# Performance work log

Measured on AMD Instinct MI355X. Metric: run time of the kernel, lower is better.

Reference implementation:

```python
import jax, jax.numpy as jnp
import numpy as np

NCHUNK, NBATCH, HALF = 32, 64, 128
C_SCALE, M_SCALE = 1e-4, 1e-5


def force(t):
    return jnp.sin(t)


def setup_inputs() -> dict:
    key = jax.random.key(0)
    k1, k2, k3, k4, k5 = jax.random.split(key, 5)
    t = jax.random.uniform(k1, (NCHUNK, NBATCH), dtype=jnp.float32)
    y = jax.random.normal(k2, (NCHUNK, NBATCH, 2 * HALF), dtype=jnp.float32)
    # positive stiffness / damping / mass, bounded away from zero
    K = jax.random.uniform(k3, (HALF,), dtype=jnp.float32) + 0.5
    C = jax.random.uniform(k4, (HALF,), dtype=jnp.float32) + 0.5
    M = jax.random.uniform(k5, (HALF,), dtype=jnp.float32) + 0.5
    return {"t": t, "y": y, "K": K, "C": C, "M": M}


def reference(t, y, K, C, M):
    half = K.shape[0]
    size = 2 * half
    Ms = M * M_SCALE
    Cs = C * C_SCALE

    u = y[..., :half]          # displacements (nchunk, nbatch, half)
    v = y[..., half:]          # velocities    (nchunk, nbatch, half)
    du = jnp.diff(u, axis=-1)  # (..., half-1)
    dv = jnp.diff(v, axis=-1)

    # internal force per link i: K_i*du_i + C_i*dv_i, distributed to nodes i and i+1
    f = K[:-1] * du + Cs[:-1] * dv                         # (..., half-1)
    pad = [(0, 0)] * (y.ndim - 1)
    vdot = jnp.pad(f / Ms[:-1], pad + [(0, 1)]) \
         + jnp.pad(-f / Ms[1:], pad + [(1, 0)])            # (..., half)
    vdot = vdot.at[..., -1].add(-(K[-1] * u[..., -1] + Cs[-1] * v[..., -1]) / Ms[-1])
    vdot = vdot.at[..., 0].add(force(t) / Ms[0])
    ydot = jnp.concatenate([v, vdot], axis=-1)             # (..., size)

    # Jacobian is constant over chunk/batch dims: assemble one (size,size) block matrix
    # lower-left block: d(vdot)/d(u)
    ku = jnp.diag(-K / Ms)
    ku = ku.at[1:, 1:].add(jnp.diag(-K[:-1] / Ms[1:]))
    ku = ku + jnp.diag(K[:-1] / Ms[:-1], k=1) + jnp.diag(K[:-1] / Ms[1:], k=-1)
    # lower-right block: d(vdot)/d(v)
    kv = jnp.diag(-Cs / Ms)
    kv = kv.at[1:, 1:].add(jnp.diag(-Cs[:-1] / Ms[1:]))
    kv = kv + jnp.diag(Cs[:-1] / Ms[:-1], k=1) + jnp.diag(Cs[:-1] / Ms[1:], k=-1)

    Jb = jnp.zeros((size, size), dtype=y.dtype)
    Jb = Jb.at[:half, half:].set(jnp.eye(half, dtype=y.dtype))  # d(udot)/d(v) = I
    Jb = Jb.at[half:, :half].set(ku)
    Jb = Jb.at[half:, half:].set(kv)

    J = jnp.broadcast_to(Jb, y.shape + (size,))
    return ydot, J
```

## Files before the change

kernel.cpp:

```cpp
#include <hip/hip_runtime.h>
#include <hip/hip_bf16.h>

#define NCHUNK 32
#define NBATCH 64
#define HALF   128
#define SIZE   (2 * HALF)
#define NROWS  (NCHUNK * NBATCH)
#define C_SCALE 1e-4f
#define M_SCALE 1e-5f

__global__ void jb_kernel(const float* __restrict__ K,
                          const float* __restrict__ C,
                          const float* __restrict__ M,
                          float* __restrict__ Jb) {
    int r = blockIdx.x;
    int c = threadIdx.x;
    float val = 0.0f;
    if (r < HALF) {
        val = (c == r + HALF) ? 1.0f : 0.0f;
    } else {
        int i = r - HALF;
        float Mi = M[i] * M_SCALE;
        bool isV = (c >= HALF);
        int  j   = isV ? (c - HALF) : c;
        float scale = isV ? C_SCALE : 1.0f;
        const float* __restrict__ A = isV ? C : K;
        if (j == i) {
            val = -A[i] * scale / Mi;
            if (i >= 1) val += -A[i - 1] * scale / Mi;
        } else if (j == i + 1 && i < HALF - 1) {
            val = A[i] * scale / Mi;
        } else if (j == i - 1) {
            val = A[i - 1] * scale / Mi;
        }
    }
    Jb[r * SIZE + c] = val;
}

__global__ void bcast_kernel(const float4* __restrict__ src,
                             float4* __restrict__ dst,
                             long total4) {
    long idx    = (long)blockIdx.x * blockDim.x + threadIdx.x;
    long stride = (long)gridDim.x * blockDim.x;
    for (; idx < total4; idx += stride) {
        dst[idx] = src[idx & 16383];
    }
}

__global__ void ydot_kernel(const float* __restrict__ t,
                            const float* __restrict__ y,
                            const float* __restrict__ K,
                            const float* __restrict__ C,
                            const float* __restrict__ M,
                            float* __restrict__ out) {
    int row = blockIdx.x;
    int i   = threadIdx.x;
    const float* yr = y + (long)row * SIZE;

    float u = yr[i];
    float v = yr[HALF + i];
    out[(long)row * SIZE + i] = v;

    float Mi   = M[i] * M_SCALE;
    float vdot = 0.0f;
    if (i < HALF - 1) {
        float f = K[i] * (yr[i + 1] - u) + C[i] * C_SCALE * (yr[HALF + i + 1] - v);
        vdot += f / Mi;
    }
    if (i >= 1) {
        float fm = K[i - 1] * (u - yr[i - 1]) + C[i - 1] * C_SCALE * (v - yr[HALF + i - 1]);
        vdot -= fm / Mi;
    }
    if (i == HALF - 1) {
        vdot += -(K[HALF - 1] * u + C[HALF - 1] * C_SCALE * v) / Mi;
    }
    if (i == 0) {
        vdot += sinf(t[row]) / Mi;
    }
    out[(long)row * SIZE + HALF + i] = vdot;
}

extern "C" void kernel_launch(void* const* d_in, const int* in_sizes, int n_in,
                              void* d_out, int out_size, void* d_ws, size_t ws_size,
                              hipStream_t stream) {
    const float* t = (const float*)d_in[0];
    const float* y = (const float*)d_in[1];
    const float* K = (const float*)d_in[2];
    const float* C = (const float*)d_in[3];
    const float* M = (const float*)d_in[4];

    float* out  = (float*)d_out;
    float* Jout = out + (long)NROWS * SIZE;

    jb_kernel<<<SIZE, SIZE, 0, stream>>>(K, C, M, Jout);

    const float4* src = (const float4*)Jout;
    float4*       dst = (float4*)Jout + 16384;
    long total4 = (long)(NROWS - 1) * 16384;
    bcast_kernel<<<2048, 256, 0, stream>>>(src, dst, total4);

    ydot_kernel<<<NROWS, HALF, 0, stream>>>(t, y, K, C, M, out);
}
```

Before: 538.9 us.

## Fuse Jacobian build and broadcast into one write-only kernel

Drops the separate Jb build kernel and the broadcast copy kernel. Each thread now computes its float4 of the block matrix in registers and writes it straight into 64 output copies, so the copy kernel's re-reads of the source block and one launch go away. The grid is 2048 blocks, each covering one 256-float4 slice across 64 copies, and every block recomputes the same Jb values redundantly. Division is replaced by multiplying with a reciprocal.

```diff
diff --git a/kernel.cpp b/kernel.cpp
--- a/kernel.cpp
+++ b/kernel.cpp
@@ -9,41 +9,54 @@
 #define C_SCALE 1e-4f
 #define M_SCALE 1e-5f
 
-__global__ void jb_kernel(const float* __restrict__ K,
-                          const float* __restrict__ C,
-                          const float* __restrict__ M,
-                          float* __restrict__ Jb) {
-    int r = blockIdx.x;
-    int c = threadIdx.x;
-    float val = 0.0f;
+#define JB_F4   16384
+#define COPIES_PER_GROUP 64
+
+__global__ __launch_bounds__(256) void j_kernel(const float* __restrict__ K,
+                                                const float* __restrict__ C,
+                                                const float* __restrict__ M,
+                                                float* __restrict__ Jout) {
+    int tid = threadIdx.x;
+    int b   = blockIdx.x;
+    int s   = b & 63;
+    int g   = b >> 6;
+    int o4  = s * 256 + tid;
+    int r   = o4 >> 6;
+    int c0  = (o4 & 63) << 2;
+
+    float vals[4];
     if (r < HALF) {
-        val = (c == r + HALF) ? 1.0f : 0.0f;
+        #pragma unroll
+        for (int k = 0; k < 4; ++k)
+            vals[k] = (c0 + k == r + HALF) ? 1.0f : 0.0f;
     } else {
-        int i = r - HALF;
-        float Mi = M[i] * M_SCALE;
-        bool isV = (c >= HALF);
-        int  j   = isV ? (c - HALF) : c;
-        float scale = isV ? C_SCALE : 1.0f;
-        const float* __restrict__ A = isV ? C : K;
-        if (j == i) {
-            val = -A[i] * scale / Mi;
-            if (i >= 1) val += -A[i - 1] * scale / Mi;
-        } else if (j == i + 1 && i < HALF - 1) {
-            val = A[i] * scale / Mi;
-        } else if (j == i - 1) {
-            val = A[i - 1] * scale / Mi;
+        int   i     = r - HALF;
+        float invMi = 1.0f / (M[i] * M_SCALE);
+        #pragma unroll
+        for (int k = 0; k < 4; ++k) {
+            int  c   = c0 + k;
+            bool isV = (c >= HALF);
+            int  j   = isV ? (c - HALF) : c;
+            float scale = isV ? C_SCALE : 1.0f;
+            const float* __restrict__ A = isV ? C : K;
+            float v = 0.0f;
+            if (j == i) {
+                v = -A[i] * scale * invMi;
+                if (i >= 1) v += -A[i - 1] * scale * invMi;
+            } else if (j == i + 1 && i < HALF - 1) {
+                v = A[i] * scale * invMi;
+            } else if (j == i - 1) {
+                v = A[i - 1] * scale * invMi;
+            }
+            vals[k] = v;
         }
     }
-    Jb[r * SIZE + c] = val;
-}
+    float4 val = make_float4(vals[0], vals[1], vals[2], vals[3]);
 
-__global__ void bcast_kernel(const float4* __restrict__ src,
-                             float4* __restrict__ dst,
-                             long total4) {
-    long idx    = (long)blockIdx.x * blockDim.x + threadIdx.x;
-    long stride = (long)gridDim.x * blockDim.x;
-    for (; idx < total4; idx += stride) {
-        dst[idx] = src[idx & 16383];
+    float4* dst = (float4*)Jout + (long)g * COPIES_PER_GROUP * JB_F4 + o4;
+    #pragma unroll
+    for (int cp = 0; cp < COPIES_PER_GROUP; ++cp) {
+        dst[(long)cp * JB_F4] = val;
     }
 }
 
@@ -92,12 +105,7 @@
     float* out  = (float*)d_out;
     float* Jout = out + (long)NROWS * SIZE;
 
-    jb_kernel<<<SIZE, SIZE, 0, stream>>>(K, C, M, Jout);
-
-    const float4* src = (const float4*)Jout;
-    float4*       dst = (float4*)Jout + 16384;
-    long total4 = (long)(NROWS - 1) * 16384;
-    bcast_kernel<<<2048, 256, 0, stream>>>(src, dst, total4);
+    j_kernel<<<NROWS, 256, 0, stream>>>(K, C, M, Jout);
 
     ydot_kernel<<<NROWS, HALF, 0, stream>>>(t, y, K, C, M, out);
 }
```

Result: no change. 531.2 us (-1.4%).

## Fuse Jacobian generation, broadcast and ydot into one write-only kernel

Applied to the files above, without the earlier changes.

Replaces the three launches (build one Jacobian block, copy it to every row, compute ydot) with a single kernel. Each block regenerates the 256x256 Jacobian directly in registers and writes it with vectorized nontemporal stores, so the broadcast no longer reads the source block, and ydot runs as extra blocks in the same grid. This removes the read traffic and launch overhead of the broadcast in exchange for recomputing the tridiagonal entries (with a division per row) in every block.

```diff
diff --git a/kernel.cpp b/kernel.cpp
--- a/kernel.cpp
+++ b/kernel.cpp
@@ -9,75 +9,85 @@
 #define C_SCALE 1e-4f
 #define M_SCALE 1e-5f
 
-__global__ void jb_kernel(const float* __restrict__ K,
-                          const float* __restrict__ C,
-                          const float* __restrict__ M,
-                          float* __restrict__ Jb) {
-    int r = blockIdx.x;
-    int c = threadIdx.x;
-    float val = 0.0f;
-    if (r < HALF) {
-        val = (c == r + HALF) ? 1.0f : 0.0f;
+#define JB_F4    16384
+#define JBLOCKS  NROWS
+#define YBLOCKS  (NROWS * HALF / 256)
+
+typedef float floatx4 __attribute__((ext_vector_type(4)));
+
+__global__ __launch_bounds__(256) void fused_kernel(
+        const float* __restrict__ t,
+        const float* __restrict__ y,
+        const float* __restrict__ K,
+        const float* __restrict__ C,
+        const float* __restrict__ M,
+        float* __restrict__ out) {
+    int b   = blockIdx.x;
+    int tid = threadIdx.x;
+
+    if (b < JBLOCKS) {
+        floatx4* dst = (floatx4*)(out + (long)NROWS * SIZE) + (long)b * JB_F4;
+        int w  = __builtin_amdgcn_readfirstlane(tid >> 6);
+        int c0 = (tid & 63) << 2;
+        bool  isV = (c0 >= HALF);
+        int   j0  = isV ? (c0 - HALF) : c0;
+        float scl = isV ? C_SCALE : 1.0f;
+        const float* __restrict__ A = isV ? C : K;
+
+        #pragma unroll
+        for (int st = 0; st < 64; ++st) {
+            int r = (st << 2) + w;
+            floatx4 val;
+            if (r < HALF) {
+                int d = r + HALF - c0;
+                val.x = (d == 0) ? 1.0f : 0.0f;
+                val.y = (d == 1) ? 1.0f : 0.0f;
+                val.z = (d == 2) ? 1.0f : 0.0f;
+                val.w = (d == 3) ? 1.0f : 0.0f;
+            } else {
+                int   i    = r - HALF;
+                float invM = 1.0f / (M[i] * M_SCALE);
+                float Ai   = A[i] * scl;
+                float Aim  = (i > 0) ? A[i - 1] * scl : 0.0f;
+                float diag = -(Ai + Aim) * invM;
+                float sup  = (i < HALF - 1) ? Ai * invM : 0.0f;
+                float sub  = Aim * invM;
+                int d = i - j0;
+                val.x = (d == 0) ? diag : (d == -1) ? sup : (d == 1) ? sub : 0.0f;
+                val.y = (d == 1) ? diag : (d ==  0) ? sup : (d == 2) ? sub : 0.0f;
+                val.z = (d == 2) ? diag : (d ==  1) ? sup : (d == 3) ? sub : 0.0f;
+                val.w = (d == 3) ? diag : (d ==  2) ? sup : (d == 4) ? sub : 0.0f;
+            }
+            __builtin_nontemporal_store(val, dst + st * 256 + tid);
+        }
     } else {
-        int i = r - HALF;
-        float Mi = M[i] * M_SCALE;
-        bool isV = (c >= HALF);
-        int  j   = isV ? (c - HALF) : c;
-        float scale = isV ? C_SCALE : 1.0f;
-        const float* __restrict__ A = isV ? C : K;
-        if (j == i) {
-            val = -A[i] * scale / Mi;
-            if (i >= 1) val += -A[i - 1] * scale / Mi;
-        } else if (j == i + 1 && i < HALF - 1) {
-            val = A[i] * scale / Mi;
-        } else if (j == i - 1) {
-            val = A[i - 1] * scale / Mi;
+        int gid = (b - JBLOCKS) * 256 + tid;
+        int row = gid >> 7;
+        int i   = gid & 127;
+        const float* yr = y + (long)row * SIZE;
+
+        float u = yr[i];
+        float v = yr[HALF + i];
+        out[(long)row * SIZE + i] = v;
+
+        float Mi   = M[i] * M_SCALE;
+        float vdot = 0.0f;
+        if (i < HALF - 1) {
+            float f = K[i] * (yr[i + 1] - u) + C[i] * C_SCALE * (yr[HALF + i + 1] - v);
+            vdot += f / Mi;
         }
+        if (i >= 1) {
+            float fm = K[i - 1] * (u - yr[i - 1]) + C[i - 1] * C_SCALE * (v - yr[HALF + i - 1]);
+            vdot -= fm / Mi;
+        }
+        if (i == HALF - 1) {
+            vdot += -(K[HALF - 1] * u + C[HALF - 1] * C_SCALE * v) / Mi;
+        }
+        if (i == 0) {
+            vdot += sinf(t[row]) / Mi;
+        }
+        out[(long)row * SIZE + HALF + i] = vdot;
     }
-    Jb[r * SIZE + c] = val;
-}
-
-__global__ void bcast_kernel(const float4* __restrict__ src,
-                             float4* __restrict__ dst,
-                             long total4) {
-    long idx    = (long)blockIdx.x * blockDim.x + threadIdx.x;
-    long stride = (long)gridDim.x * blockDim.x;
-    for (; idx < total4; idx += stride) {
-        dst[idx] = src[idx & 16383];
-    }
-}
-
-__global__ void ydot_kernel(const float* __restrict__ t,
-                            const float* __restrict__ y,
-                            const float* __restrict__ K,
-                            const float* __restrict__ C,
-                            const float* __restrict__ M,
-                            float* __restrict__ out) {
-    int row = blockIdx.x;
-    int i   = threadIdx.x;
-    const float* yr = y + (long)row * SIZE;
-
-    float u = yr[i];
-    float v = yr[HALF + i];
-    out[(long)row * SIZE + i] = v;
-
-    float Mi   = M[i] * M_SCALE;
-    float vdot = 0.0f;
-    if (i < HALF - 1) {
-        float f = K[i] * (yr[i + 1] - u) + C[i] * C_SCALE * (yr[HALF + i + 1] - v);
-        vdot += f / Mi;
-    }
-    if (i >= 1) {
-        float fm = K[i - 1] * (u - yr[i - 1]) + C[i - 1] * C_SCALE * (v - yr[HALF + i - 1]);
-        vdot -= fm / Mi;
-    }
-    if (i == HALF - 1) {
-        vdot += -(K[HALF - 1] * u + C[HALF - 1] * C_SCALE * v) / Mi;
-    }
-    if (i == 0) {
-        vdot += sinf(t[row]) / Mi;
-    }
-    out[(long)row * SIZE + HALF + i] = vdot;
 }
 
 extern "C" void kernel_launch(void* const* d_in, const int* in_sizes, int n_in,
@@ -89,15 +99,7 @@
     const float* C = (const float*)d_in[3];
     const float* M = (const float*)d_in[4];
 
-    float* out  = (float*)d_out;
-    float* Jout = out + (long)NROWS * SIZE;
+    float* out = (float*)d_out;
 
-    jb_kernel<<<SIZE, SIZE, 0, stream>>>(K, C, M, Jout);
-
-    const float4* src = (const float4*)Jout;
-    float4*       dst = (float4*)Jout + 16384;
-    long total4 = (long)(NROWS - 1) * 16384;
-    bcast_kernel<<<2048, 256, 0, stream>>>(src, dst, total4);
-
-    ydot_kernel<<<NROWS, HALF, 0, stream>>>(t, y, K, C, M, out);
+    fused_kernel<<<JBLOCKS + YBLOCKS, 256, 0, stream>>>(t, y, K, C, M, out);
 }
```

Measured after the change: 532.1 us. About the same (-1.2%).
